# Optimization experiments

Hardware: AMD Instinct MI355X
Metric: run time of the kernel (lower is better)

## Reference

```python
import jax, jax.numpy as jnp
import numpy as np
from jax import lax

N, C_IN, C_OUT, T, V = 16, 256, 256, 300, 25
K = 3            # s_kernel_size
TK = 9           # t_kernel_size
BN_EPS = 1e-5


def setup_inputs() -> dict:
    key = jax.random.key(0)
    ks = jax.random.split(key, 12)
    x = jax.random.normal(ks[0], (N, C_IN, T, V), dtype=jnp.float32)
    A = jax.random.uniform(ks[1], (K, V, V), dtype=jnp.float32)
    att_A = jax.random.uniform(ks[2], (N, 1, V, V), dtype=jnp.float32)  # unused by S_GC
    M = jnp.ones((K, V, V), dtype=jnp.float32)
    # 1x1 spatial conv: out = K*C_OUT channels
    conv_w = jax.random.normal(ks[3], (K * C_OUT, C_IN), dtype=jnp.float32) * 0.02
    conv_b = jnp.zeros((K * C_OUT,), dtype=jnp.float32)
    # BN1 (eval mode)
    bn1_gamma = jnp.ones((C_OUT,), dtype=jnp.float32)
    bn1_beta = jnp.zeros((C_OUT,), dtype=jnp.float32)
    bn1_mean = jax.random.normal(ks[4], (C_OUT,), dtype=jnp.float32) * 0.1
    bn1_var = jax.random.uniform(ks[5], (C_OUT,), dtype=jnp.float32) + 0.5
    # temporal conv: kernel (TK, 1), stride 1, pad ((TK-1)//2, 0)
    tconv_w = jax.random.normal(ks[6], (C_OUT, C_OUT, TK, 1), dtype=jnp.float32) * 0.02
    tconv_b = jnp.zeros((C_OUT,), dtype=jnp.float32)
    # BN2 (eval mode)
    bn2_gamma = jnp.ones((C_OUT,), dtype=jnp.float32)
    bn2_beta = jnp.zeros((C_OUT,), dtype=jnp.float32)
    bn2_mean = jax.random.normal(ks[7], (C_OUT,), dtype=jnp.float32) * 0.1
    bn2_var = jax.random.uniform(ks[8], (C_OUT,), dtype=jnp.float32) + 0.5
    return {
        "x": x, "A": A, "att_A": att_A, "M": M,
        "conv_w": conv_w, "conv_b": conv_b,
        "bn1_gamma": bn1_gamma, "bn1_beta": bn1_beta, "bn1_mean": bn1_mean, "bn1_var": bn1_var,
        "tconv_w": tconv_w, "tconv_b": tconv_b,
        "bn2_gamma": bn2_gamma, "bn2_beta": bn2_beta, "bn2_mean": bn2_mean, "bn2_var": bn2_var,
    }


def _bn(x, gamma, beta, mean, var):
    # eval-mode BatchNorm2d over channel dim of NCHW tensor
    scale = gamma / jnp.sqrt(var + BN_EPS)
    return x * scale[None, :, None, None] + (beta - mean * scale)[None, :, None, None]


def reference(x, A, att_A, M, conv_w, conv_b,
              bn1_gamma, bn1_beta, bn1_mean, bn1_var,
              tconv_w, tconv_b,
              bn2_gamma, bn2_beta, bn2_mean, bn2_var):
    # --- S_GC: 1x1 conv -> view (n,K,c,t,v) -> einsum with A*M ---
    y = jnp.einsum('nctv,oc->notv', x, conv_w) + conv_b[None, :, None, None]
    y = y.reshape(N, K, C_OUT, T, V)
    sgc = jnp.einsum('nkctv,kvw->nctw', y, A * M)
    # --- tgc: BN -> ReLU -> temporal conv -> BN -> Dropout(0) -> ReLU ---
    h = jax.nn.relu(_bn(sgc, bn1_gamma, bn1_beta, bn1_mean, bn1_var))
    h = lax.conv_general_dilated(
        h, tconv_w, window_strides=(1, 1),
        padding=(((TK - 1) // 2, (TK - 1) // 2), (0, 0)),
        dimension_numbers=('NCHW', 'OIHW', 'NCHW'))
    h = h + tconv_b[None, :, None, None]
    h = jax.nn.relu(_bn(h, bn2_gamma, bn2_beta, bn2_mean, bn2_var))
    # --- residual: identity (in_channels == out_channels, stride == 1) ---
    return h + x
```

## Files before the change

kernel.cpp:

```cpp
#include <hip/hip_runtime.h>
#include <math.h>

constexpr int TVL = 7500;
constexpr int CIN = 256;
constexpr int CO  = 256;
constexpr int KO  = 768;
constexpr int KK3 = 2304;
#define BNEPS 1e-5f

typedef __attribute__((ext_vector_type(8))) short short8;
typedef __attribute__((ext_vector_type(4))) float f32x4;
typedef unsigned short ushortT;

static __device__ __forceinline__ ushortT f2bf(float v) {
    unsigned x = __float_as_uint(v);
    unsigned r = (x + 0x7fffu + ((x >> 16) & 1u)) >> 16;
    return (ushortT)r;
}
static __device__ __forceinline__ float bf2f(ushortT u) {
    return __uint_as_float((unsigned)u << 16);
}

static __device__ __forceinline__ void gll16(const void* g, void* l) {
    __builtin_amdgcn_global_load_lds(
        (const __attribute__((address_space(1))) void*)g,
        (__attribute__((address_space(3))) void*)l, 16, 0, 0);
}

static __device__ __forceinline__ void xcd_remap(int gx, int gy,
                                                 int& bx, int& by, int& bz)
{
    const int gz = gridDim.z;
    const int total = gx * gy * gz;
    const int lin = blockIdx.x + gx * (blockIdx.y + gy * blockIdx.z);
    const int q = total >> 3, r = total & 7;
    const int xcd = lin & 7, idx = lin >> 3;
    const int nl = (xcd < r ? xcd * (q + 1) : r * (q + 1) + (xcd - r) * q) + idx;
    bx = nl % gx;
    const int rest = nl / gx;
    by = rest % gy;
    bz = rest / gy;
}

__global__ void ksplit_w1(const float* __restrict__ w,
                          ushortT* __restrict__ dH, ushortT* __restrict__ dL,
                          ushortT* __restrict__ zb)
{
    if (blockIdx.x == 0 && threadIdx.x < 16) zb[threadIdx.x] = 0;
    int i = blockIdx.x * 256 + threadIdx.x;
    if (i < KO * CIN) {
        float v = w[i];
        ushortT h = f2bf(v);
        dH[i] = h;
        dL[i] = f2bf(v - bf2f(h));
    }
}

__global__ void ksplit_w3(const float* __restrict__ w,
                          ushortT* __restrict__ dH, ushortT* __restrict__ dL)
{
    int i = blockIdx.x * 256 + threadIdx.x;
    if (i < CO * KK3) {
        int o = i / KK3, rem = i - o * KK3;
        int c = rem / 9, dt = rem - c * 9;
        float v = w[i];
        ushortT h = f2bf(v);
        int j = o * KK3 + dt * 256 + c;
        dH[j] = h;
        dL[j] = f2bf(v - bf2f(h));
    }
}

__global__ __launch_bounds__(256) void ktrans_split(
    const float* __restrict__ src, size_t zstr,
    ushortT* __restrict__ dH, ushortT* __restrict__ dL)
{
    __shared__ float tile[32][33];
    const int z = blockIdx.z;
    src += (size_t)z * zstr;
    dH  += (size_t)z * TVL * 256;
    dL  += (size_t)z * TVL * 256;
    const int tx = threadIdx.x & 31, ty = threadIdx.x >> 5;
    const int wBase = blockIdx.x * 32, cBase = blockIdx.y * 32;
    #pragma unroll
    for (int i = 0; i < 4; ++i) {
        int r = ty + i * 8;
        int w = wBase + tx;
        tile[r][tx] = (w < TVL) ? src[(size_t)(cBase + r) * TVL + w] : 0.f;
    }
    __syncthreads();
    #pragma unroll
    for (int i = 0; i < 4; ++i) {
        int wr = ty + i * 8;
        int w = wBase + wr;
        if (w < TVL) {
            float v = tile[tx][wr];
            ushortT hi = f2bf(v);
            ushortT lo = f2bf(v - bf2f(hi));
            dH[(size_t)w * 256 + cBase + tx] = hi;
            dL[(size_t)w * 256 + cBase + tx] = lo;
        }
    }
}

__global__ __launch_bounds__(256) void k1_mfma(
    const ushortT* __restrict__ Wh, const ushortT* __restrict__ Wl,
    const ushortT* __restrict__ Xh, const ushortT* __restrict__ Xl,
    const ushortT* __restrict__ zb,
    const float* __restrict__ bias, float* __restrict__ out1)
{
    __shared__ __align__(16) short Ah[2][4096], Al[2][4096], Bh[2][4096], Bl[2][4096];
    const int tid = threadIdx.x;
    int bx, by, bz;
    xcd_remap(gridDim.x, gridDim.y, bx, by, bz);
    const int ng = bz;
    const int rowBase = by * 128;
    const int colBase = bx * 128;
    const ushortT* XhN = Xh + (size_t)ng * TVL * 256;
    const ushortT* XlN = Xl + (size_t)ng * TVL * 256;

    f32x4 acc[4][4];
    #pragma unroll
    for (int a = 0; a < 4; ++a)
        #pragma unroll
        for (int b = 0; b < 4; ++b) acc[a][b] = (f32x4){0.f, 0.f, 0.f, 0.f};

    const int r0 = tid >> 2, s = tid & 3;
    const int wv = tid >> 6, lane = tid & 63;
    const int wy = wv >> 1, wx = wv & 1;
    const int q = lane >> 4, l15 = lane & 15;
    const int qs0 = s ^ ((r0 >> 1) & 3);
    const int qsr = q ^ ((l15 >> 1) & 3);
    const int ldo0 = tid * 16, ldo1 = 4096 + tid * 16;
    const int bcol0 = colBase + r0, bcol1 = colBase + r0 + 64;

    auto stage = [&](int kk, int p) {
        short* ahp = Ah[p]; short* alp = Al[p];
        short* bhp = Bh[p]; short* blp = Bl[p];
        const size_t goA = (size_t)(rowBase + r0) * CIN + kk + qs0 * 8;
        gll16(Wh + goA, (char*)ahp + ldo0);
        gll16(Wl + goA, (char*)alp + ldo0);
        gll16(Wh + goA + (size_t)64 * CIN, (char*)ahp + ldo1);
        gll16(Wl + goA + (size_t)64 * CIN, (char*)alp + ldo1);
        const size_t goB0 = (size_t)bcol0 * 256 + kk + qs0 * 8;
        const size_t goB1 = (size_t)bcol1 * 256 + kk + qs0 * 8;
        gll16(bcol0 < TVL ? (const void*)(XhN + goB0) : (const void*)zb, (char*)bhp + ldo0);
        gll16(bcol0 < TVL ? (const void*)(XlN + goB0) : (const void*)zb, (char*)blp + ldo0);
        gll16(bcol1 < TVL ? (const void*)(XhN + goB1) : (const void*)zb, (char*)bhp + ldo1);
        gll16(bcol1 < TVL ? (const void*)(XlN + goB1) : (const void*)zb, (char*)blp + ldo1);
    };

    stage(0, 0);
    __syncthreads();
    int p = 0;

    #pragma unroll 1
    for (int kk = 0; kk < CIN; kk += 32) {
        if (kk + 32 < CIN) stage(kk + 32, p ^ 1);

        const char* AhP = (const char*)Ah[p];
        const char* AlP = (const char*)Al[p];
        const char* BhP = (const char*)Bh[p];
        const char* BlP = (const char*)Bl[p];
        short8 ah[4], al[4], bh[4], bl[4];
        #pragma unroll
        for (int mi = 0; mi < 4; ++mi) {
            const int off = (wy * 64 + mi * 16 + l15) * 64 + qsr * 16;
            ah[mi] = *(const short8*)(AhP + off);
            al[mi] = *(const short8*)(AlP + off);
        }
        #pragma unroll
        for (int ni = 0; ni < 4; ++ni) {
            const int off = (wx * 64 + ni * 16 + l15) * 64 + qsr * 16;
            bh[ni] = *(const short8*)(BhP + off);
            bl[ni] = *(const short8*)(BlP + off);
        }
        #pragma unroll
        for (int mi = 0; mi < 4; ++mi)
            #pragma unroll
            for (int ni = 0; ni < 4; ++ni) {
                acc[mi][ni] = __builtin_amdgcn_mfma_f32_16x16x32_bf16(ah[mi], bh[ni], acc[mi][ni], 0, 0, 0);
                acc[mi][ni] = __builtin_amdgcn_mfma_f32_16x16x32_bf16(ah[mi], bl[ni], acc[mi][ni], 0, 0, 0);
                acc[mi][ni] = __builtin_amdgcn_mfma_f32_16x16x32_bf16(al[mi], bh[ni], acc[mi][ni], 0, 0, 0);
            }
        __syncthreads();
        p ^= 1;
    }

    float* out1n = out1 + (size_t)ng * KO * TVL;
    #pragma unroll
    for (int mi = 0; mi < 4; ++mi)
        #pragma unroll
        for (int rr = 0; rr < 4; ++rr) {
            const int row = rowBase + wy * 64 + mi * 16 + q * 4 + rr;
            const float bv = bias[row];
            #pragma unroll
            for (int ni = 0; ni < 4; ++ni) {
                const int col = colBase + wx * 64 + ni * 16 + l15;
                if (col < TVL)
                    out1n[(size_t)row * TVL + col] = acc[mi][ni][rr] + bv;
            }
        }
}

__global__ __launch_bounds__(256) void k2_sgc(
    const float* out1, const float* __restrict__ A,
    const float* __restrict__ Mm, const float* __restrict__ g1,
    const float* __restrict__ b1, const float* __restrict__ m1,
    const float* __restrict__ v1, float* h)
{
    __shared__ __align__(16) float AMs[3 * 25 * 28];
    const int tid = threadIdx.x;
    for (int i = tid; i < 1875; i += 256)
        AMs[(i / 25) * 28 + (i % 25)] = A[i] * Mm[i];
    __syncthreads();

    const int r  = blockIdx.x * 256 + tid;
    const int t2 = r % 150;
    const int rc = r / 150;
    const int c  = rc & 255;
    const int ng = rc >> 8;
    const int t  = t2 * 2;

    const float* base = out1 + ((size_t)ng * KO + c) * TVL + t * 25;
    float o0[25], o1[25];
    #pragma unroll
    for (int w = 0; w < 25; ++w) { o0[w] = 0.f; o1[w] = 0.f; }

    for (int k = 0; k < 3; ++k) {
        const float* yp = base + (size_t)k * CO * TVL;
        float y0[25], y1[25];
        #pragma unroll
        for (int v = 0; v < 25; ++v) { y0[v] = yp[v]; y1[v] = yp[25 + v]; }
        const float* amk = &AMs[k * 25 * 28];
        for (int v = 0; v < 25; ++v) {
            const float* am = amk + v * 28;
            const float ya = y0[v], yb = y1[v];
            #pragma unroll
            for (int w = 0; w < 25; ++w) {
                const float a = am[w];
                o0[w] += ya * a;
                o1[w] += yb * a;
            }
        }
    }

    const float sc = g1[c] / sqrtf(v1[c] + BNEPS);
    const float bi = b1[c] - m1[c] * sc;
    float* hp = h + ((size_t)ng * KO + c) * TVL + t * 25;
    #pragma unroll
    for (int w = 0; w < 25; ++w) {
        const float va = o0[w] * sc + bi;
        const float vb = o1[w] * sc + bi;
        hp[w]      = va > 0.f ? va : 0.f;
        hp[25 + w] = vb > 0.f ? vb : 0.f;
    }
}

__global__ __launch_bounds__(256) void k3_mfma(
    const ushortT* __restrict__ Wh, const ushortT* __restrict__ Wl,
    const ushortT* __restrict__ Hh, const ushortT* __restrict__ Hl,
    const ushortT* __restrict__ zb,
    const float* __restrict__ tb, const float* __restrict__ g2,
    const float* __restrict__ b2, const float* __restrict__ m2,
    const float* __restrict__ v2, const float* __restrict__ x,
    float* __restrict__ out, int n0)
{
    __shared__ __align__(16) short Ah[2][4096], Al[2][4096], Bh[2][4096], Bl[2][4096];
    const int tid = threadIdx.x;
    int bx, by, bz;
    xcd_remap(gridDim.x, gridDim.y, bx, by, bz);
    const int ng = bz;
    const int rowBase = by * 128;
    const int colBase = bx * 128;
    const ushortT* HhN = Hh + (size_t)ng * TVL * 256;
    const ushortT* HlN = Hl + (size_t)ng * TVL * 256;

    f32x4 acc[4][4];
    #pragma unroll
    for (int a = 0; a < 4; ++a)
        #pragma unroll
        for (int b = 0; b < 4; ++b) acc[a][b] = (f32x4){0.f, 0.f, 0.f, 0.f};

    const int r0 = tid >> 2, s = tid & 3;
    const int wv = tid >> 6, lane = tid & 63;
    const int wy = wv >> 1, wx = wv & 1;
    const int q = lane >> 4, l15 = lane & 15;
    const int qs0 = s ^ ((r0 >> 1) & 3);
    const int qsr = q ^ ((l15 >> 1) & 3);
    const int ldo0 = tid * 16, ldo1 = 4096 + tid * 16;
    const int bcol0 = colBase + r0, bcol1 = colBase + r0 + 64;

    auto stage = [&](int kk, int p) {
        short* ahp = Ah[p]; short* alp = Al[p];
        short* bhp = Bh[p]; short* blp = Bl[p];
        const int dt = kk >> 8;
        const int c0 = kk & 255;
        const int shift = dt * 25 - 100;
        const size_t goA = (size_t)(rowBase + r0) * KK3 + kk + qs0 * 8;
        gll16(Wh + goA, (char*)ahp + ldo0);
        gll16(Wl + goA, (char*)alp + ldo0);
        gll16(Wh + goA + (size_t)64 * KK3, (char*)ahp + ldo1);
        gll16(Wl + goA + (size_t)64 * KK3, (char*)alp + ldo1);
        const int gcol0 = bcol0 + shift, gcol1 = bcol1 + shift;
        const bool ok0 = (bcol0 < TVL) && ((unsigned)gcol0 < (unsigned)TVL);
        const bool ok1 = (bcol1 < TVL) && ((unsigned)gcol1 < (unsigned)TVL);
        const size_t goB0 = (size_t)gcol0 * 256 + c0 + qs0 * 8;
        const size_t goB1 = (size_t)gcol1 * 256 + c0 + qs0 * 8;
        gll16(ok0 ? (const void*)(HhN + goB0) : (const void*)zb, (char*)bhp + ldo0);
        gll16(ok0 ? (const void*)(HlN + goB0) : (const void*)zb, (char*)blp + ldo0);
        gll16(ok1 ? (const void*)(HhN + goB1) : (const void*)zb, (char*)bhp + ldo1);
        gll16(ok1 ? (const void*)(HlN + goB1) : (const void*)zb, (char*)blp + ldo1);
    };

    stage(0, 0);
    __syncthreads();
    int p = 0;

    #pragma unroll 1
    for (int kk = 0; kk < KK3; kk += 32) {
        if (kk + 32 < KK3) stage(kk + 32, p ^ 1);

        const char* AhP = (const char*)Ah[p];
        const char* AlP = (const char*)Al[p];
        const char* BhP = (const char*)Bh[p];
        const char* BlP = (const char*)Bl[p];
        short8 ah[4], al[4], bh[4], bl[4];
        #pragma unroll
        for (int mi = 0; mi < 4; ++mi) {
            const int off = (wy * 64 + mi * 16 + l15) * 64 + qsr * 16;
            ah[mi] = *(const short8*)(AhP + off);
            al[mi] = *(const short8*)(AlP + off);
        }
        #pragma unroll
        for (int ni = 0; ni < 4; ++ni) {
            const int off = (wx * 64 + ni * 16 + l15) * 64 + qsr * 16;
            bh[ni] = *(const short8*)(BhP + off);
            bl[ni] = *(const short8*)(BlP + off);
        }
        #pragma unroll
        for (int mi = 0; mi < 4; ++mi)
            #pragma unroll
            for (int ni = 0; ni < 4; ++ni) {
                acc[mi][ni] = __builtin_amdgcn_mfma_f32_16x16x32_bf16(ah[mi], bh[ni], acc[mi][ni], 0, 0, 0);
                acc[mi][ni] = __builtin_amdgcn_mfma_f32_16x16x32_bf16(ah[mi], bl[ni], acc[mi][ni], 0, 0, 0);
                acc[mi][ni] = __builtin_amdgcn_mfma_f32_16x16x32_bf16(al[mi], bh[ni], acc[mi][ni], 0, 0, 0);
            }
        __syncthreads();
        p ^= 1;
    }

    const float* xn = x   + (size_t)(n0 + ng) * CO * TVL;
    float*       on = out + (size_t)(n0 + ng) * CO * TVL;
    #pragma unroll
    for (int mi = 0; mi < 4; ++mi)
        #pragma unroll
        for (int rr = 0; rr < 4; ++rr) {
            const int row = rowBase + wy * 64 + mi * 16 + q * 4 + rr;
            const float sc = g2[row] / sqrtf(v2[row] + BNEPS);
            const float bb = (tb[row] - m2[row]) * sc + b2[row];
            #pragma unroll
            for (int ni = 0; ni < 4; ++ni) {
                const int col = colBase + wx * 64 + ni * 16 + l15;
                if (col < TVL) {
                    const size_t o = (size_t)row * TVL + col;
                    on[o] = fmaxf(acc[mi][ni][rr] * sc + bb, 0.f) + xn[o];
                }
            }
        }
}

extern "C" void kernel_launch(void* const* d_in, const int* in_sizes, int n_in,
                              void* d_out, int out_size, void* d_ws, size_t ws_size,
                              hipStream_t stream)
{
    const float* x  = (const float*)d_in[0];
    const float* A  = (const float*)d_in[1];
    const float* Mm = (const float*)d_in[3];
    const float* cw = (const float*)d_in[4];
    const float* cb = (const float*)d_in[5];
    const float* g1 = (const float*)d_in[6];
    const float* b1 = (const float*)d_in[7];
    const float* m1 = (const float*)d_in[8];
    const float* v1 = (const float*)d_in[9];
    const float* tw = (const float*)d_in[10];
    const float* tb = (const float*)d_in[11];
    const float* g2 = (const float*)d_in[12];
    const float* b2 = (const float*)d_in[13];
    const float* m2 = (const float*)d_in[14];
    const float* v2 = (const float*)d_in[15];
    float* out = (float*)d_out;

    ushortT* zb  = (ushortT*)d_ws;
    ushortT* W1h = (ushortT*)((char*)d_ws + 256);
    ushortT* W1l = W1h + KO * CIN;
    ushortT* W3h = W1l + KO * CIN;
    ushortT* W3l = W3h + CO * KK3;
    char* dyn = (char*)(W3l + CO * KK3);
    const size_t fixed = (size_t)(dyn - (char*)d_ws);
    const size_t avail = ws_size > fixed ? ws_size - fixed : 0;
    const size_t perN = (size_t)KO * TVL * 4 + 2 * (size_t)TVL * 256 * 2;
    int g = 16;
    while (g > 1 && (size_t)g * perN > avail) g >>= 1;

    float*   out1 = (float*)dyn;
    ushortT* Xh   = (ushortT*)(out1 + (size_t)g * KO * TVL);
    ushortT* Xl   = Xh + (size_t)g * TVL * 256;

    hipLaunchKernelGGL(ksplit_w1, dim3((KO * CIN + 255) / 256), dim3(256), 0, stream, cw, W1h, W1l, zb);
    hipLaunchKernelGGL(ksplit_w3, dim3((CO * KK3 + 255) / 256), dim3(256), 0, stream, tw, W3h, W3l);

    for (int n0 = 0; n0 < 16; n0 += g) {
        hipLaunchKernelGGL(ktrans_split, dim3(235, 8, g), dim3(256), 0, stream,
                           x + (size_t)n0 * CIN * TVL, (size_t)CIN * TVL, Xh, Xl);
        hipLaunchKernelGGL(k1_mfma, dim3(59, 6, g), dim3(256), 0, stream,
                           W1h, W1l, Xh, Xl, zb, cb, out1);
        hipLaunchKernelGGL(k2_sgc, dim3(g * 150), dim3(256), 0, stream,
                           out1, A, Mm, g1, b1, m1, v1, out1 );
        hipLaunchKernelGGL(ktrans_split, dim3(235, 8, g), dim3(256), 0, stream,
                           out1, (size_t)KO * TVL, Xh, Xl);
        hipLaunchKernelGGL(k3_mfma, dim3(59, 2, g), dim3(256), 0, stream,
                           W3h, W3l, Xh, Xl, zb, tb, g2, b2, m2, v2, x, out, n0);
    }
}
```

Baseline: 1.250 ms.

## Load weight fragments directly from global into registers, halve LDS usage

In both MFMA GEMM kernels the A-operand (weight hi/lo) tiles are no longer staged through shared memory. Each wave now reads its weight fragments straight from global memory (L2/L1-cached) into registers at the top of each k-step. Only the activation B tiles stay in double-buffered LDS. Launch bounds are raised to request 3 blocks per CU, since LDS per block is halved. The intent is higher occupancy and fewer LDS writes and reads. The risk is exposed global-load latency on the weights, because those loads are issued right before use without prefetching.

Result: slower. 1.559 ms (+24.7%).

```diff
diff --git a/kernel.cpp b/kernel.cpp
--- a/kernel.cpp
+++ b/kernel.cpp
@@ -103,13 +103,13 @@
     }
 }
 
-__global__ __launch_bounds__(256) void k1_mfma(
+__global__ __launch_bounds__(256, 3) void k1_mfma(
     const ushortT* __restrict__ Wh, const ushortT* __restrict__ Wl,
     const ushortT* __restrict__ Xh, const ushortT* __restrict__ Xl,
     const ushortT* __restrict__ zb,
     const float* __restrict__ bias, float* __restrict__ out1)
 {
-    __shared__ __align__(16) short Ah[2][4096], Al[2][4096], Bh[2][4096], Bl[2][4096];
+    __shared__ __align__(16) short Bh[2][4096], Bl[2][4096];
     const int tid = threadIdx.x;
     int bx, by, bz;
     xcd_remap(gridDim.x, gridDim.y, bx, by, bz);
@@ -134,14 +134,11 @@
     const int ldo0 = tid * 16, ldo1 = 4096 + tid * 16;
     const int bcol0 = colBase + r0, bcol1 = colBase + r0 + 64;
 
-    auto stage = [&](int kk, int p) {
-        short* ahp = Ah[p]; short* alp = Al[p];
+    const ushortT* WhR = Wh + (size_t)(rowBase + wy * 64 + l15) * CIN + q * 8;
+    const ushortT* WlR = Wl + (size_t)(rowBase + wy * 64 + l15) * CIN + q * 8;
+
+    auto stageB = [&](int kk, int p) {
         short* bhp = Bh[p]; short* blp = Bl[p];
-        const size_t goA = (size_t)(rowBase + r0) * CIN + kk + qs0 * 8;
-        gll16(Wh + goA, (char*)ahp + ldo0);
-        gll16(Wl + goA, (char*)alp + ldo0);
-        gll16(Wh + goA + (size_t)64 * CIN, (char*)ahp + ldo1);
-        gll16(Wl + goA + (size_t)64 * CIN, (char*)alp + ldo1);
         const size_t goB0 = (size_t)bcol0 * 256 + kk + qs0 * 8;
         const size_t goB1 = (size_t)bcol1 * 256 + kk + qs0 * 8;
         gll16(bcol0 < TVL ? (const void*)(XhN + goB0) : (const void*)zb, (char*)bhp + ldo0);
@@ -150,25 +147,23 @@
         gll16(bcol1 < TVL ? (const void*)(XlN + goB1) : (const void*)zb, (char*)blp + ldo1);
     };
 
-    stage(0, 0);
+    stageB(0, 0);
     __syncthreads();
     int p = 0;
 
     #pragma unroll 1
     for (int kk = 0; kk < CIN; kk += 32) {
-        if (kk + 32 < CIN) stage(kk + 32, p ^ 1);
-
-        const char* AhP = (const char*)Ah[p];
-        const char* AlP = (const char*)Al[p];
+        short8 ah[4], al[4];
+        #pragma unroll
+        for (int mi = 0; mi < 4; ++mi) {
+            ah[mi] = *(const short8*)(WhR + (size_t)mi * 16 * CIN + kk);
+            al[mi] = *(const short8*)(WlR + (size_t)mi * 16 * CIN + kk);
+        }
+        if (kk + 32 < CIN) stageB(kk + 32, p ^ 1);
+
         const char* BhP = (const char*)Bh[p];
         const char* BlP = (const char*)Bl[p];
-        short8 ah[4], al[4], bh[4], bl[4];
-        #pragma unroll
-        for (int mi = 0; mi < 4; ++mi) {
-            const int off = (wy * 64 + mi * 16 + l15) * 64 + qsr * 16;
-            ah[mi] = *(const short8*)(AhP + off);
-            al[mi] = *(const short8*)(AlP + off);
-        }
+        short8 bh[4], bl[4];
         #pragma unroll
         for (int ni = 0; ni < 4; ++ni) {
             const int off = (wx * 64 + ni * 16 + l15) * 64 + qsr * 16;
@@ -257,7 +252,7 @@
     }
 }
 
-__global__ __launch_bounds__(256) void k3_mfma(
+__global__ __launch_bounds__(256, 3) void k3_mfma(
     const ushortT* __restrict__ Wh, const ushortT* __restrict__ Wl,
     const ushortT* __restrict__ Hh, const ushortT* __restrict__ Hl,
     const ushortT* __restrict__ zb,
@@ -266,7 +261,7 @@
     const float* __restrict__ v2, const float* __restrict__ x,
     float* __restrict__ out, int n0)
 {
-    __shared__ __align__(16) short Ah[2][4096], Al[2][4096], Bh[2][4096], Bl[2][4096];
+    __shared__ __align__(16) short Bh[2][4096], Bl[2][4096];
     const int tid = threadIdx.x;
     int bx, by, bz;
     xcd_remap(gridDim.x, gridDim.y, bx, by, bz);
@@ -291,17 +286,14 @@
     const int ldo0 = tid * 16, ldo1 = 4096 + tid * 16;
     const int bcol0 = colBase + r0, bcol1 = colBase + r0 + 64;
 
-    auto stage = [&](int kk, int p) {
-        short* ahp = Ah[p]; short* alp = Al[p];
+    const ushortT* WhR = Wh + (size_t)(rowBase + wy * 64 + l15) * KK3 + q * 8;
+    const ushortT* WlR = Wl + (size_t)(rowBase + wy * 64 + l15) * KK3 + q * 8;
+
+    auto stageB = [&](int kk, int p) {
         short* bhp = Bh[p]; short* blp = Bl[p];
         const int dt = kk >> 8;
         const int c0 = kk & 255;
         const int shift = dt * 25 - 100;
-        const size_t goA = (size_t)(rowBase + r0) * KK3 + kk + qs0 * 8;
-        gll16(Wh + goA, (char*)ahp + ldo0);
-        gll16(Wl + goA, (char*)alp + ldo0);
-        gll16(Wh + goA + (size_t)64 * KK3, (char*)ahp + ldo1);
-        gll16(Wl + goA + (size_t)64 * KK3, (char*)alp + ldo1);
         const int gcol0 = bcol0 + shift, gcol1 = bcol1 + shift;
         const bool ok0 = (bcol0 < TVL) && ((unsigned)gcol0 < (unsigned)TVL);
         const bool ok1 = (bcol1 < TVL) && ((unsigned)gcol1 < (unsigned)TVL);
@@ -313,25 +305,23 @@
         gll16(ok1 ? (const void*)(HlN + goB1) : (const void*)zb, (char*)blp + ldo1);
     };
 
-    stage(0, 0);
+    stageB(0, 0);
     __syncthreads();
     int p = 0;
 
     #pragma unroll 1
     for (int kk = 0; kk < KK3; kk += 32) {
-        if (kk + 32 < KK3) stage(kk + 32, p ^ 1);
-
-        const char* AhP = (const char*)Ah[p];
-        const char* AlP = (const char*)Al[p];
+        short8 ah[4], al[4];
+        #pragma unroll
+        for (int mi = 0; mi < 4; ++mi) {
+            ah[mi] = *(const short8*)(WhR + (size_t)mi * 16 * KK3 + kk);
+            al[mi] = *(const short8*)(WlR + (size_t)mi * 16 * KK3 + kk);
+        }
+        if (kk + 32 < KK3) stageB(kk + 32, p ^ 1);
+
         const char* BhP = (const char*)Bh[p];
         const char* BlP = (const char*)Bl[p];
-        short8 ah[4], al[4], bh[4], bl[4];
-        #pragma unroll
-        for (int mi = 0; mi < 4; ++mi) {
-            const int off = (wy * 64 + mi * 16 + l15) * 64 + qsr * 16;
-            ah[mi] = *(const short8*)(AhP + off);
-            al[mi] = *(const short8*)(AlP + off);
-        }
+        short8 bh[4], bl[4];
         #pragma unroll
         for (int ni = 0; ni < 4; ++ni) {
             const int off = (wx * 64 + ni * 16 + l15) * 64 + qsr * 16;
```

## Reuse a haloed activation strip across all temporal taps in the tconv GEMM

Applied to the files above, without the earlier changes.

The temporal-conv MFMA kernel now iterates channel chunks in the outer loop and the 9 temporal offsets in the inner loop. For each 32-channel chunk it stages a 384-column activation strip once (the 128 output columns plus a ±100 halo) into LDS and reads shifted windows from it for every tap. Before, a shifted B tile was reloaded from global memory for each tap. Only the weight tiles stay double-buffered. The strip load is not prefetched and waits on a barrier, and LDS use rises, which may lower occupancy.

New measurement: 1.206 ms. 3.6% less time.

```diff
diff --git a/kernel.cpp b/kernel.cpp
--- a/kernel.cpp
+++ b/kernel.cpp
@@ -46,7 +46,7 @@
                           ushortT* __restrict__ dH, ushortT* __restrict__ dL,
                           ushortT* __restrict__ zb)
 {
-    if (blockIdx.x == 0 && threadIdx.x < 16) zb[threadIdx.x] = 0;
+    if (blockIdx.x == 0 && threadIdx.x < 128) zb[threadIdx.x] = 0;
     int i = blockIdx.x * 256 + threadIdx.x;
     if (i < KO * CIN) {
         float v = w[i];
@@ -266,7 +266,8 @@
     const float* __restrict__ v2, const float* __restrict__ x,
     float* __restrict__ out, int n0)
 {
-    __shared__ __align__(16) short Ah[2][4096], Al[2][4096], Bh[2][4096], Bl[2][4096];
+    __shared__ __align__(16) short Sh[384 * 32], Sl[384 * 32];
+    __shared__ __align__(16) short Ah[2][4096], Al[2][4096];
     const int tid = threadIdx.x;
     int bx, by, bz;
     xcd_remap(gridDim.x, gridDim.y, bx, by, bz);
@@ -289,65 +290,73 @@
     const int qs0 = s ^ ((r0 >> 1) & 3);
     const int qsr = q ^ ((l15 >> 1) & 3);
     const int ldo0 = tid * 16, ldo1 = 4096 + tid * 16;
-    const int bcol0 = colBase + r0, bcol1 = colBase + r0 + 64;
-
-    auto stage = [&](int kk, int p) {
+
+    auto stageStrip = [&](int c0) {
+        #pragma unroll
+        for (int i = 0; i < 6; ++i) {
+            const int gcol = colBase - 128 + i * 64 + r0;
+            const bool ok = (unsigned)gcol < (unsigned)TVL;
+            const size_t go = (size_t)gcol * 256 + c0 + qs0 * 8;
+            gll16(ok ? (const void*)(HhN + go) : (const void*)zb,
+                  (char*)Sh + i * 4096 + tid * 16);
+            gll16(ok ? (const void*)(HlN + go) : (const void*)zb,
+                  (char*)Sl + i * 4096 + tid * 16);
+        }
+    };
+    auto stageA = [&](int kp, int p) {
         short* ahp = Ah[p]; short* alp = Al[p];
-        short* bhp = Bh[p]; short* blp = Bl[p];
-        const int dt = kk >> 8;
-        const int c0 = kk & 255;
-        const int shift = dt * 25 - 100;
-        const size_t goA = (size_t)(rowBase + r0) * KK3 + kk + qs0 * 8;
+        const size_t goA = (size_t)(rowBase + r0) * KK3 + kp + qs0 * 8;
         gll16(Wh + goA, (char*)ahp + ldo0);
         gll16(Wl + goA, (char*)alp + ldo0);
         gll16(Wh + goA + (size_t)64 * KK3, (char*)ahp + ldo1);
         gll16(Wl + goA + (size_t)64 * KK3, (char*)alp + ldo1);
-        const int gcol0 = bcol0 + shift, gcol1 = bcol1 + shift;
-        const bool ok0 = (bcol0 < TVL) && ((unsigned)gcol0 < (unsigned)TVL);
-        const bool ok1 = (bcol1 < TVL) && ((unsigned)gcol1 < (unsigned)TVL);
-        const size_t goB0 = (size_t)gcol0 * 256 + c0 + qs0 * 8;
-        const size_t goB1 = (size_t)gcol1 * 256 + c0 + qs0 * 8;
-        gll16(ok0 ? (const void*)(HhN + goB0) : (const void*)zb, (char*)bhp + ldo0);
-        gll16(ok0 ? (const void*)(HlN + goB0) : (const void*)zb, (char*)blp + ldo0);
-        gll16(ok1 ? (const void*)(HhN + goB1) : (const void*)zb, (char*)bhp + ldo1);
-        gll16(ok1 ? (const void*)(HlN + goB1) : (const void*)zb, (char*)blp + ldo1);
     };
 
-    stage(0, 0);
-    __syncthreads();
+    stageA(0, 0);
     int p = 0;
 
     #pragma unroll 1
-    for (int kk = 0; kk < KK3; kk += 32) {
-        if (kk + 32 < KK3) stage(kk + 32, p ^ 1);
-
-        const char* AhP = (const char*)Ah[p];
-        const char* AlP = (const char*)Al[p];
-        const char* BhP = (const char*)Bh[p];
-        const char* BlP = (const char*)Bl[p];
-        short8 ah[4], al[4], bh[4], bl[4];
-        #pragma unroll
-        for (int mi = 0; mi < 4; ++mi) {
-            const int off = (wy * 64 + mi * 16 + l15) * 64 + qsr * 16;
-            ah[mi] = *(const short8*)(AhP + off);
-            al[mi] = *(const short8*)(AlP + off);
-        }
-        #pragma unroll
-        for (int ni = 0; ni < 4; ++ni) {
-            const int off = (wx * 64 + ni * 16 + l15) * 64 + qsr * 16;
-            bh[ni] = *(const short8*)(BhP + off);
-            bl[ni] = *(const short8*)(BlP + off);
-        }
-        #pragma unroll
-        for (int mi = 0; mi < 4; ++mi)
+    for (int cc = 0; cc < 8; ++cc) {
+        const int c0 = cc * 32;
+        stageStrip(c0);
+        __syncthreads();
+
+        #pragma unroll 1
+        for (int dt = 0; dt < 9; ++dt) {
+            {
+                int ndt = dt + 1, nc0 = c0;
+                if (ndt == 9) { ndt = 0; nc0 += 32; }
+                if (nc0 < 256) stageA(ndt * 256 + nc0, p ^ 1);
+            }
+
+            const char* AhP = (const char*)Ah[p];
+            const char* AlP = (const char*)Al[p];
+            short8 ah[4], al[4], bh[4], bl[4];
+            #pragma unroll
+            for (int mi = 0; mi < 4; ++mi) {
+                const int off = (wy * 64 + mi * 16 + l15) * 64 + qsr * 16;
+                ah[mi] = *(const short8*)(AhP + off);
+                al[mi] = *(const short8*)(AlP + off);
+            }
+            const int sbase = wx * 64 + dt * 25 + 28;
             #pragma unroll
             for (int ni = 0; ni < 4; ++ni) {
-                acc[mi][ni] = __builtin_amdgcn_mfma_f32_16x16x32_bf16(ah[mi], bh[ni], acc[mi][ni], 0, 0, 0);
-                acc[mi][ni] = __builtin_amdgcn_mfma_f32_16x16x32_bf16(ah[mi], bl[ni], acc[mi][ni], 0, 0, 0);
-                acc[mi][ni] = __builtin_amdgcn_mfma_f32_16x16x32_bf16(al[mi], bh[ni], acc[mi][ni], 0, 0, 0);
-            }
-        __syncthreads();
-        p ^= 1;
+                const int sc = sbase + ni * 16 + l15;
+                const int off = sc * 64 + ((q ^ ((sc >> 1) & 3)) << 4);
+                bh[ni] = *(const short8*)((const char*)Sh + off);
+                bl[ni] = *(const short8*)((const char*)Sl + off);
+            }
+            #pragma unroll
+            for (int mi = 0; mi < 4; ++mi)
+                #pragma unroll
+                for (int ni = 0; ni < 4; ++ni) {
+                    acc[mi][ni] = __builtin_amdgcn_mfma_f32_16x16x32_bf16(ah[mi], bh[ni], acc[mi][ni], 0, 0, 0);
+                    acc[mi][ni] = __builtin_amdgcn_mfma_f32_16x16x32_bf16(ah[mi], bl[ni], acc[mi][ni], 0, 0, 0);
+                    acc[mi][ni] = __builtin_amdgcn_mfma_f32_16x16x32_bf16(al[mi], bh[ni], acc[mi][ni], 0, 0, 0);
+                }
+            __syncthreads();
+            p ^= 1;
+        }
     }
 
     const float* xn = x   + (size_t)(n0 + ng) * CO * TVL;
```
